# Optimization experiments

Hardware: AMD Instinct MI355X
Metric: run time of the kernel (lower is better)

Reference implementation:

```python
import jax, jax.numpy as jnp
import numpy as np

BN_EPS = 1e-5


def setup_inputs() -> dict:
    key = jax.random.key(0)
    ks = jax.random.split(key, 9)
    C = 256
    x = jax.random.normal(ks[0], (4, C, 56, 56), jnp.float32)
    Wq = jax.random.normal(ks[1], (C // 4, C), jnp.float32) * 0.05
    Wk = jax.random.normal(ks[2], (C // 4, C), jnp.float32) * 0.05
    Wv = jax.random.normal(ks[3], (C, 2 * C), jnp.float32) * 0.05
    bv = jax.random.normal(ks[4], (C,), jnp.float32) * 0.05
    gamma = jnp.ones((C,), jnp.float32)
    beta = jnp.zeros((C,), jnp.float32)
    rmean = jax.random.normal(ks[5], (C,), jnp.float32) * 0.05
    rvar = jax.random.uniform(ks[6], (C,), jnp.float32) + 0.5
    return {"x": x, "Wq": Wq, "Wk": Wk, "Wv": Wv, "bv": bv,
            "gamma": gamma, "beta": beta, "rmean": rmean, "rvar": rvar, "k": 7}


def _patches(t, k):
    # t: [b, c, h, w] -> [b, c, k*k, h, w], zero-padded neighborhoods (matches F.unfold row-major order)
    b, c, h, w = t.shape
    p = (k - 1) // 2
    tp = jnp.pad(t, ((0, 0), (0, 0), (p, p), (p, p)))
    return jnp.stack([tp[:, :, i:i + h, j:j + w] for i in range(k) for j in range(k)], axis=2)


def _align(ta, tb, k, Wq, Wk):
    b, c, h, w = ta.shape
    hw = h * w
    # query token per pixel: [b, hw, 1, c]
    spta = ta.reshape(b, c, hw).transpose(0, 2, 1)[:, :, None, :]
    # unfolded k^2 neighborhood of tb: [b, hw, k2, c]
    pt = _patches(tb, k).reshape(b, c, k * k, hw).transpose(0, 3, 2, 1)
    keys = jnp.concatenate([spta, pt], axis=2)          # [b, hw, 1+k2, c]
    q = jnp.einsum('bnqc,dc->bnqd', spta, Wq)           # [b, hw, 1, c/4]
    kk = jnp.einsum('bnkc,dc->bnkd', keys, Wk)          # [b, hw, 1+k2, c/4]
    attn = jax.nn.softmax(jnp.einsum('bnqd,bnkd->bnqk', q, kk), axis=-1)
    out = jnp.einsum('bnqk,bnkc->bnqc', attn[..., 1:], pt)  # drop self-key column
    return out[:, :, 0, :].transpose(0, 2, 1).reshape(b, c, h, w)


def reference(x, Wq, Wk, Wv, bv, gamma, beta, rmean, rvar, k):
    xt1, xt2 = jnp.split(x, 2, axis=0)
    xt1 = _align(xt2, xt1, k, Wq, Wk)   # note: second call uses the freshly aligned xt1 (as in source)
    xt2 = _align(xt1, xt2, k, Wq, Wk)
    xt = jnp.concatenate([xt1, xt2], axis=0)
    cat = jnp.concatenate([x, xt], axis=1)              # [2B, 2C, H, W]
    y = jnp.einsum('bchw,oc->bohw', cat, Wv) + bv[None, :, None, None]
    scale = (gamma / jnp.sqrt(rvar + BN_EPS))[None, :, None, None]
    y = (y - rmean[None, :, None, None]) * scale + beta[None, :, None, None]
    return jax.nn.relu(y)
```

## Files before the change

### kernel.cpp

```cpp
#include <hip/hip_runtime.h>
#include <hip/hip_bf16.h>

#define HW 3136
#define W56 56

typedef __attribute__((ext_vector_type(8))) short short8;
typedef __attribute__((ext_vector_type(4))) float f32x4;

static __device__ __forceinline__ f32x4 mfma16(short8 a, short8 b, f32x4 c) {
    return __builtin_amdgcn_mfma_f32_16x16x32_bf16(a, b, c, 0, 0, 0);
}
static __device__ __forceinline__ float b2f(unsigned short u) {
    unsigned int x = ((unsigned int)u) << 16;
    return __builtin_bit_cast(float, x);
}
static __device__ __forceinline__ unsigned short f2b(float f) {
    __hip_bfloat16 h = __float2bfloat16(f);
    return *(unsigned short*)&h;
}

__global__ __launch_bounds__(256) void prep(const float* __restrict__ x,
                                            const float* __restrict__ Wq, const float* __restrict__ Wk,
                                            const float* __restrict__ Wv,
                                            unsigned short* __restrict__ catb,
                                            unsigned short* __restrict__ xlo,
                                            unsigned short* __restrict__ Wqk_hi,
                                            unsigned short* __restrict__ Wqk_lo,
                                            unsigned short* __restrict__ Wvb) {
    __shared__ float tile[32][33];
    int bx = blockIdx.x, tid = threadIdx.x;
    if (bx < 3136) {
        int b = bx / 784, rem = bx % 784;
        int p0 = (rem >> 3) * 32, c0 = (rem & 7) * 32;
        int tx = tid & 31, ty = tid >> 5;
#pragma unroll
        for (int i = ty; i < 32; i += 8)
            tile[i][tx] = x[((size_t)b * 256 + c0 + i) * HW + p0 + tx];
        __syncthreads();
#pragma unroll
        for (int i = ty; i < 32; i += 8) {
            float v = tile[tx][i];
            unsigned short hi = f2b(v);
            unsigned short lo = f2b(v - b2f(hi));
            size_t row = (size_t)b * HW + p0 + i;
            catb[row * 512 + c0 + tx] = hi;
            xlo[row * 256 + c0 + tx] = lo;
        }
    } else {
        int i = (bx - 3136) * 256 + tid;
        if (i < 32768) {
            float w = (i < 16384) ? Wq[i] : Wk[i - 16384];
            unsigned short hi = f2b(w);
            Wqk_hi[i] = hi;
            Wqk_lo[i] = f2b(w - b2f(hi));
        }
        if (i < 131072) Wvb[i] = f2b(Wv[i]);
    }
}

__global__ __launch_bounds__(256) void projqk(const unsigned short* __restrict__ Whi,
                                              const unsigned short* __restrict__ Wlo,
                                              const unsigned short* __restrict__ Bhi_g, int bstr,
                                              const unsigned short* __restrict__ Blo_g,
                                              float* __restrict__ Qout,
                                              unsigned short* __restrict__ Kout) {
    __shared__ short Ahi[64][72], Alo[64][72];
    __shared__ short Bhi[32][72], Blo[32][72];
    int tid = threadIdx.x, lane = tid & 63, wv = tid >> 6;
    int l15 = lane & 15, lk = (lane >> 4) * 8;
    int pxb = blockIdx.x * 32;
    int y64 = blockIdx.y * 64;
    int ar0 = tid >> 3, ac = (tid & 7) * 8;
    int br = tid >> 3, bc = (tid & 7) * 8;
    f32x4 acc[2];
    acc[0] = (f32x4){0.f, 0.f, 0.f, 0.f};
    acc[1] = (f32x4){0.f, 0.f, 0.f, 0.f};

    short8 rAh0 = *(const short8*)(Whi + (size_t)(y64 + ar0) * 256 + ac);
    short8 rAl0 = *(const short8*)(Wlo + (size_t)(y64 + ar0) * 256 + ac);
    short8 rAh1 = *(const short8*)(Whi + (size_t)(y64 + ar0 + 32) * 256 + ac);
    short8 rAl1 = *(const short8*)(Wlo + (size_t)(y64 + ar0 + 32) * 256 + ac);
    short8 rBh  = *(const short8*)(Bhi_g + (size_t)(pxb + br) * bstr + bc);
    short8 rBl  = *(const short8*)(Blo_g + (size_t)(pxb + br) * 256 + bc);

#pragma unroll
    for (int t = 0; t < 4; ++t) {
        *(short8*)&Ahi[ar0][ac] = rAh0;      *(short8*)&Alo[ar0][ac] = rAl0;
        *(short8*)&Ahi[ar0 + 32][ac] = rAh1; *(short8*)&Alo[ar0 + 32][ac] = rAl1;
        *(short8*)&Bhi[br][bc] = rBh;        *(short8*)&Blo[br][bc] = rBl;
        __syncthreads();
        if (t < 3) {
            int kn = t * 64 + 64;
            rAh0 = *(const short8*)(Whi + (size_t)(y64 + ar0) * 256 + kn + ac);
            rAl0 = *(const short8*)(Wlo + (size_t)(y64 + ar0) * 256 + kn + ac);
            rAh1 = *(const short8*)(Whi + (size_t)(y64 + ar0 + 32) * 256 + kn + ac);
            rAl1 = *(const short8*)(Wlo + (size_t)(y64 + ar0 + 32) * 256 + kn + ac);
            rBh  = *(const short8*)(Bhi_g + (size_t)(pxb + br) * bstr + kn + bc);
            rBl  = *(const short8*)(Blo_g + (size_t)(pxb + br) * 256 + kn + bc);
        }
#pragma unroll
        for (int ks = 0; ks < 2; ++ks) {
            short8 ah = *(const short8*)&Ahi[wv * 16 + l15][ks * 32 + lk];
            short8 al = *(const short8*)&Alo[wv * 16 + l15][ks * 32 + lk];
            short8 bh[2], bl[2];
#pragma unroll
            for (int j = 0; j < 2; ++j) {
                bh[j] = *(const short8*)&Bhi[j * 16 + l15][ks * 32 + lk];
                bl[j] = *(const short8*)&Blo[j * 16 + l15][ks * 32 + lk];
            }
#pragma unroll
            for (int j = 0; j < 2; ++j) {
                acc[j] = mfma16(ah, bh[j], acc[j]);
                acc[j] = mfma16(ah, bl[j], acc[j]);
                acc[j] = mfma16(al, bh[j], acc[j]);
            }
        }
        __syncthreads();
    }
    int d0 = wv * 16 + (lane >> 4) * 4;
    if (blockIdx.y == 0) {
#pragma unroll
        for (int j = 0; j < 2; ++j) {
            int px = pxb + j * 16 + l15;
            *(f32x4*)(Qout + (size_t)px * 64 + d0) = acc[j];
        }
    } else {
#pragma unroll
        for (int j = 0; j < 2; ++j) {
            int px = pxb + j * 16 + l15;
            ushort4 kb;
            kb.x = f2b(acc[j][0]); kb.y = f2b(acc[j][1]);
            kb.z = f2b(acc[j][2]); kb.w = f2b(acc[j][3]);
            *(ushort4*)(Kout + (size_t)px * 64 + d0) = kb;
        }
    }
}

__global__ __launch_bounds__(256) void attn_kernel(const float* __restrict__ Q,
                                                   const unsigned short* __restrict__ Kb,
                                                   int selfOff, int kbOff,
                                                   const unsigned short* __restrict__ V,
                                                   unsigned short* __restrict__ outb,
                                                   unsigned short* __restrict__ outlo) {
    __shared__ float wsh[4][64];
    __shared__ float ls[4][52];
    __shared__ int njsh[4][64];
    int tid = threadIdx.x, lane = tid & 63, wv = tid >> 6;
    int nbc = gridDim.x >> 3;
    int lb = (blockIdx.x & 7) * nbc + (blockIdx.x >> 3);
    int gw = lb * 4 + wv;
    int b = gw / HW, pix = gw % HW;
    int py = pix / W56, px = pix % W56;

    int valid = 0, nj = 0;
    if (lane == 0) {
        valid = 1;
    } else if (lane < 50) {
        int d = lane - 1, dy = d / 7 - 3, dx = d % 7 - 3;
        int ny = py + dy, nx = px + dx;
        if (ny >= 0 && ny < W56 && nx >= 0 && nx < W56) { valid = 1; nj = ny * W56 + nx; }
    }
    njsh[wv][lane] = nj;

    int rg = lane >> 4, c = lane & 15;
    f32x4 qf = *(const f32x4*)(Q + (size_t)gw * 64 + c * 4);
    ushort4 kvv[13];
#pragma unroll
    for (int i = 0; i < 13; ++i) {
        int r = i * 4 + rg;
        int row = (i == 0 && rg == 0) ? (selfOff + gw) : (kbOff + b * HW + njsh[wv][r]);
        kvv[i] = *(const ushort4*)(Kb + (size_t)row * 64 + c * 4);
    }

    float pl[13];
#pragma unroll
    for (int i = 0; i < 13; ++i)
        pl[i] = b2f(kvv[i].x) * qf[0] + b2f(kvv[i].y) * qf[1] +
                b2f(kvv[i].z) * qf[2] + b2f(kvv[i].w) * qf[3];
#pragma unroll
    for (int off = 1; off < 16; off <<= 1)
#pragma unroll
        for (int i = 0; i < 13; ++i) pl[i] += __shfl_xor(pl[i], off);
    float myl = 0.f;
#pragma unroll
    for (int i = 0; i < 13; ++i) myl = (c == i) ? pl[i] : myl;
    if (c < 13) ls[wv][c * 4 + rg] = myl;

    float logit = (lane < 50 && valid) ? ls[wv][lane] : 0.f;
    float m = (lane < 50) ? logit : -1e30f;
#pragma unroll
    for (int off = 32; off; off >>= 1) m = fmaxf(m, __shfl_xor(m, off));
    float e = (lane < 50) ? __expf(logit - m) : 0.f;
    float s = e;
#pragma unroll
    for (int off = 32; off; off >>= 1) s += __shfl_xor(s, off);
    float w = (lane >= 1 && lane < 50 && valid) ? e / s : 0.f;
    wsh[wv][lane] = w;

    int h = lane >> 5, l32 = lane & 31;
    int jb = h * 25;
    float av[8];
#pragma unroll
    for (int cc = 0; cc < 8; ++cc) av[cc] = 0.f;
    const unsigned short* vb = V + (size_t)b * HW * 512 + l32 * 8;
#pragma unroll
    for (int g = 0; g < 2; ++g) {
        float wj[12];
        short8 vj[12];
#pragma unroll
        for (int u = 0; u < 12; ++u) {
            int j = jb + g * 12 + u;
            wj[u] = wsh[wv][j];
            vj[u] = *(const short8*)(vb + (size_t)njsh[wv][j] * 512);
        }
#pragma unroll
        for (int u = 0; u < 12; ++u)
#pragma unroll
            for (int cc = 0; cc < 8; ++cc)
                av[cc] += wj[u] * b2f((unsigned short)vj[u][cc]);
    }
    {
        int j = jb + 24;
        float wt = wsh[wv][j];
        short8 vt = *(const short8*)(vb + (size_t)njsh[wv][j] * 512);
#pragma unroll
        for (int cc = 0; cc < 8; ++cc) av[cc] += wt * b2f((unsigned short)vt[cc]);
    }
#pragma unroll
    for (int cc = 0; cc < 8; ++cc) av[cc] += __shfl_xor(av[cc], 32);

    if (h == 0) {
        short8 pk, lo8;
#pragma unroll
        for (int cc = 0; cc < 8; ++cc) {
            unsigned short hi = f2b(av[cc]);
            pk[cc] = (short)hi;
            lo8[cc] = (short)f2b(av[cc] - b2f(hi));
        }
        *(short8*)(outb + (size_t)gw * 512 + l32 * 8) = pk;
        if (outlo) *(short8*)(outlo + (size_t)gw * 256 + l32 * 8) = lo8;
    }
}

__global__ __launch_bounds__(256) void conv_mfma(const unsigned short* __restrict__ catb,
                                                 const unsigned short* __restrict__ Wvb,
                                                 const float* __restrict__ bv, const float* __restrict__ gamma,
                                                 const float* __restrict__ beta, const float* __restrict__ rmean,
                                                 const float* __restrict__ rvar, float* __restrict__ out) {
    __shared__ short Ald[64][72];
    __shared__ short Bld[64][72];
    int tid = threadIdx.x, lane = tid & 63, wv = tid >> 6;
    int wm = wv >> 1, wn = wv & 1;
    int l15 = lane & 15, lk = (lane >> 4) * 8;
    int n0g = blockIdx.x * 64;
    int m0g = blockIdx.y * 64;
    f32x4 acc[2][2];
#pragma unroll
    for (int i = 0; i < 2; ++i)
#pragma unroll
        for (int j = 0; j < 2; ++j) acc[i][j] = (f32x4){0.f, 0.f, 0.f, 0.f};

    float sc_[2][4], sh_[2][4];
#pragma unroll
    for (int i = 0; i < 2; ++i) {
        int ob = m0g + wm * 32 + i * 16 + (lane >> 4) * 4;
#pragma unroll
        for (int r = 0; r < 4; ++r) {
            int o = ob + r;
            float s = gamma[o] * rsqrtf(rvar[o] + 1e-5f);
            sc_[i][r] = s;
            sh_[i][r] = (bv[o] - rmean[o]) * s + beta[o];
        }
    }

    for (int kt = 0; kt < 512; kt += 64) {
#pragma unroll
        for (int s = 0; s < 2; ++s) {
            int q = tid + 256 * s;
            int r = q >> 3, c = (q & 7) * 8;
            *(short8*)&Ald[r][c] = *(const short8*)(Wvb + (size_t)(m0g + r) * 512 + kt + c);
            *(short8*)&Bld[r][c] = *(const short8*)(catb + (size_t)(n0g + r) * 512 + kt + c);
        }
        __syncthreads();
#pragma unroll
        for (int ks = 0; ks < 2; ++ks) {
            short8 a[2], b[2];
#pragma unroll
            for (int i = 0; i < 2; ++i) a[i] = *(const short8*)&Ald[wm * 32 + i * 16 + l15][ks * 32 + lk];
#pragma unroll
            for (int j = 0; j < 2; ++j) b[j] = *(const short8*)&Bld[wn * 32 + j * 16 + l15][ks * 32 + lk];
#pragma unroll
            for (int i = 0; i < 2; ++i)
#pragma unroll
                for (int j = 0; j < 2; ++j) acc[i][j] = mfma16(a[i], b[j], acc[i][j]);
        }
        __syncthreads();
    }
#pragma unroll
    for (int i = 0; i < 2; ++i) {
        int ob = m0g + wm * 32 + i * 16 + (lane >> 4) * 4;
#pragma unroll
        for (int j = 0; j < 2; ++j) {
            int px = n0g + wn * 32 + j * 16 + l15;
            int b = px / HW, p = px - b * HW;
            f32x4 v = acc[i][j];
#pragma unroll
            for (int r = 0; r < 4; ++r) {
                out[((size_t)(b * 256 + ob + r)) * HW + p] = fmaxf(v[r] * sc_[i][r] + sh_[i][r], 0.f);
            }
        }
    }
}

extern "C" void kernel_launch(void* const* d_in, const int* in_sizes, int n_in,
                              void* d_out, int out_size, void* d_ws, size_t ws_size,
                              hipStream_t stream) {
    const float* x     = (const float*)d_in[0];
    const float* Wq    = (const float*)d_in[1];
    const float* Wk    = (const float*)d_in[2];
    const float* Wv    = (const float*)d_in[3];
    const float* bv    = (const float*)d_in[4];
    const float* gamma = (const float*)d_in[5];
    const float* beta  = (const float*)d_in[6];
    const float* rmean = (const float*)d_in[7];
    const float* rvar  = (const float*)d_in[8];
    float* out = (float*)d_out;

    float* Qall = (float*)d_ws;
    float* Qn   = Qall + (size_t)4 * HW * 64;
    unsigned short* Kb = (unsigned short*)(Qn + (size_t)2 * HW * 64);
    unsigned short* catb   = Kb + (size_t)6 * HW * 64;
    unsigned short* xlo    = catb + (size_t)4 * HW * 512;
    unsigned short* xt1lo  = xlo + (size_t)4 * HW * 256;
    unsigned short* Wqk_hi = xt1lo + (size_t)2 * HW * 256;
    unsigned short* Wqk_lo = Wqk_hi + 128 * 256;
    unsigned short* Wvb    = Wqk_lo + 128 * 256;

    prep<<<3648, 256, 0, stream>>>(x, Wq, Wk, Wv, catb, xlo, Wqk_hi, Wqk_lo, Wvb);

    projqk<<<dim3(392, 2), 256, 0, stream>>>(Wqk_hi, Wqk_lo, catb, 512, xlo, Qall, Kb);

    attn_kernel<<<1568, 256, 0, stream>>>(Qall + (size_t)2 * HW * 64, Kb,
                                          2 * HW, 0,
                                          catb, catb + 256, xt1lo);

    projqk<<<dim3(196, 2), 256, 0, stream>>>(Wqk_hi, Wqk_lo, catb + 256, 512, xt1lo,
                                             Qn, Kb + (size_t)4 * HW * 64);

    attn_kernel<<<1568, 256, 0, stream>>>(Qn, Kb,
                                          4 * HW, 2 * HW,
                                          catb + (size_t)2 * HW * 512,
                                          catb + (size_t)2 * HW * 512 + 256, nullptr);

    conv_mfma<<<dim3(196, 4), 256, 0, stream>>>(catb, Wvb, bv, gamma, beta, rmean, rvar, out);
}
```

Baseline: 62.90 us.

## Process two adjacent pixels per wave in attention and prefetch conv tiles

The attention kernel now handles two horizontally adjacent pixels per wavefront. It builds a shared 7x8 union neighborhood, so each V row is loaded once and accumulated into both outputs with separately shifted weights. This roughly halves the gather traffic for the value aggregation and halves the grid size, at the cost of more registers and LDS. The conv GEMM also gains register prefetch of the next K tile while MFMAs run on the current one, overlapping global loads with compute.

```diff
diff --git a/kernel.cpp b/kernel.cpp
--- a/kernel.cpp
+++ b/kernel.cpp
@@ -142,104 +142,148 @@
                                                    const unsigned short* __restrict__ V,
                                                    unsigned short* __restrict__ outb,
                                                    unsigned short* __restrict__ outlo) {
-    __shared__ float wsh[4][64];
-    __shared__ float ls[4][52];
-    __shared__ int njsh[4][64];
+    __shared__ float wsh[4][2][64];
+    __shared__ float ls[4][2][52];
+    __shared__ int njs[4][2][64];
+    __shared__ int njU[4][64];
+    __shared__ float wU[4][2][64];
     int tid = threadIdx.x, lane = tid & 63, wv = tid >> 6;
     int nbc = gridDim.x >> 3;
     int lb = (blockIdx.x & 7) * nbc + (blockIdx.x >> 3);
-    int gw = lb * 4 + wv;
-    int b = gw / HW, pix = gw % HW;
-    int py = pix / W56, px = pix % W56;
-
-    int valid = 0, nj = 0;
+    int pg = lb * 8 + wv * 2;
+    int b = pg / HW, pix = pg % HW;
+    int py = pix / W56, px0 = pix % W56;
+    int gw0 = pg, gw1 = pg + 1;
+
+    int v0 = 0, n0 = 0, v1 = 0, n1 = 0;
     if (lane == 0) {
-        valid = 1;
+        v0 = 1; v1 = 1;
     } else if (lane < 50) {
         int d = lane - 1, dy = d / 7 - 3, dx = d % 7 - 3;
-        int ny = py + dy, nx = px + dx;
-        if (ny >= 0 && ny < W56 && nx >= 0 && nx < W56) { valid = 1; nj = ny * W56 + nx; }
-    }
-    njsh[wv][lane] = nj;
+        int ny = py + dy;
+        if (ny >= 0 && ny < W56) {
+            int nx0 = px0 + dx, nx1 = px0 + 1 + dx;
+            if (nx0 >= 0 && nx0 < W56) { v0 = 1; n0 = ny * W56 + nx0; }
+            if (nx1 >= 0 && nx1 < W56) { v1 = 1; n1 = ny * W56 + nx1; }
+        }
+    }
+    njs[wv][0][lane] = n0;
+    njs[wv][1][lane] = n1;
 
     int rg = lane >> 4, c = lane & 15;
-    f32x4 qf = *(const f32x4*)(Q + (size_t)gw * 64 + c * 4);
-    ushort4 kvv[13];
+    f32x4 qf0 = *(const f32x4*)(Q + (size_t)gw0 * 64 + c * 4);
+    f32x4 qf1 = *(const f32x4*)(Q + (size_t)gw1 * 64 + c * 4);
+    ushort4 kv0[13], kv1[13];
 #pragma unroll
     for (int i = 0; i < 13; ++i) {
         int r = i * 4 + rg;
-        int row = (i == 0 && rg == 0) ? (selfOff + gw) : (kbOff + b * HW + njsh[wv][r]);
-        kvv[i] = *(const ushort4*)(Kb + (size_t)row * 64 + c * 4);
-    }
-
-    float pl[13];
-#pragma unroll
-    for (int i = 0; i < 13; ++i)
-        pl[i] = b2f(kvv[i].x) * qf[0] + b2f(kvv[i].y) * qf[1] +
-                b2f(kvv[i].z) * qf[2] + b2f(kvv[i].w) * qf[3];
+        int row0 = (i == 0 && rg == 0) ? (selfOff + gw0) : (kbOff + b * HW + njs[wv][0][r]);
+        int row1 = (i == 0 && rg == 0) ? (selfOff + gw1) : (kbOff + b * HW + njs[wv][1][r]);
+        kv0[i] = *(const ushort4*)(Kb + (size_t)row0 * 64 + c * 4);
+        kv1[i] = *(const ushort4*)(Kb + (size_t)row1 * 64 + c * 4);
+    }
+
+    float pl0[13], pl1[13];
+#pragma unroll
+    for (int i = 0; i < 13; ++i) {
+        pl0[i] = b2f(kv0[i].x) * qf0[0] + b2f(kv0[i].y) * qf0[1] +
+                 b2f(kv0[i].z) * qf0[2] + b2f(kv0[i].w) * qf0[3];
+        pl1[i] = b2f(kv1[i].x) * qf1[0] + b2f(kv1[i].y) * qf1[1] +
+                 b2f(kv1[i].z) * qf1[2] + b2f(kv1[i].w) * qf1[3];
+    }
 #pragma unroll
     for (int off = 1; off < 16; off <<= 1)
 #pragma unroll
-        for (int i = 0; i < 13; ++i) pl[i] += __shfl_xor(pl[i], off);
-    float myl = 0.f;
-#pragma unroll
-    for (int i = 0; i < 13; ++i) myl = (c == i) ? pl[i] : myl;
-    if (c < 13) ls[wv][c * 4 + rg] = myl;
-
-    float logit = (lane < 50 && valid) ? ls[wv][lane] : 0.f;
-    float m = (lane < 50) ? logit : -1e30f;
-#pragma unroll
-    for (int off = 32; off; off >>= 1) m = fmaxf(m, __shfl_xor(m, off));
-    float e = (lane < 50) ? __expf(logit - m) : 0.f;
-    float s = e;
-#pragma unroll
-    for (int off = 32; off; off >>= 1) s += __shfl_xor(s, off);
-    float w = (lane >= 1 && lane < 50 && valid) ? e / s : 0.f;
-    wsh[wv][lane] = w;
+        for (int i = 0; i < 13; ++i) {
+            pl0[i] += __shfl_xor(pl0[i], off);
+            pl1[i] += __shfl_xor(pl1[i], off);
+        }
+    float my0 = 0.f, my1 = 0.f;
+#pragma unroll
+    for (int i = 0; i < 13; ++i) {
+        my0 = (c == i) ? pl0[i] : my0;
+        my1 = (c == i) ? pl1[i] : my1;
+    }
+    if (c < 13) {
+        ls[wv][0][c * 4 + rg] = my0;
+        ls[wv][1][c * 4 + rg] = my1;
+    }
+
+    float lg0 = (lane < 50 && v0) ? ls[wv][0][lane] : 0.f;
+    float lg1 = (lane < 50 && v1) ? ls[wv][1][lane] : 0.f;
+    float m0 = (lane < 50) ? lg0 : -1e30f;
+    float m1 = (lane < 50) ? lg1 : -1e30f;
+#pragma unroll
+    for (int off = 32; off; off >>= 1) {
+        m0 = fmaxf(m0, __shfl_xor(m0, off));
+        m1 = fmaxf(m1, __shfl_xor(m1, off));
+    }
+    float e0 = (lane < 50) ? __expf(lg0 - m0) : 0.f;
+    float e1 = (lane < 50) ? __expf(lg1 - m1) : 0.f;
+    float s0 = e0, s1 = e1;
+#pragma unroll
+    for (int off = 32; off; off >>= 1) {
+        s0 += __shfl_xor(s0, off);
+        s1 += __shfl_xor(s1, off);
+    }
+    wsh[wv][0][lane] = (lane >= 1 && lane < 50 && v0) ? e0 / s0 : 0.f;
+    wsh[wv][1][lane] = (lane >= 1 && lane < 50 && v1) ? e1 / s1 : 0.f;
+
+    if (lane < 56) {
+        int dy = (lane >> 3) - 3, ux = (lane & 7) - 3;
+        int ny = py + dy, nxu = px0 + ux;
+        int uv = (ny >= 0 && ny < W56 && nxu >= 0 && nxu < W56);
+        njU[wv][lane] = uv ? ny * W56 + nxu : 0;
+        float a0 = 0.f, a1 = 0.f;
+        if (ux <= 3) a0 = wsh[wv][0][1 + (dy + 3) * 7 + (ux + 3)];
+        if (ux >= -2) a1 = wsh[wv][1][1 + (dy + 3) * 7 + (ux + 2)];
+        wU[wv][0][lane] = a0;
+        wU[wv][1][lane] = a1;
+    }
 
     int h = lane >> 5, l32 = lane & 31;
-    int jb = h * 25;
-    float av[8];
-#pragma unroll
-    for (int cc = 0; cc < 8; ++cc) av[cc] = 0.f;
+    int rb = h * 28;
+    float av0[8], av1[8];
+#pragma unroll
+    for (int cc = 0; cc < 8; ++cc) { av0[cc] = 0.f; av1[cc] = 0.f; }
     const unsigned short* vb = V + (size_t)b * HW * 512 + l32 * 8;
 #pragma unroll
-    for (int g = 0; g < 2; ++g) {
-        float wj[12];
-        short8 vj[12];
-#pragma unroll
-        for (int u = 0; u < 12; ++u) {
-            int j = jb + g * 12 + u;
-            wj[u] = wsh[wv][j];
-            vj[u] = *(const short8*)(vb + (size_t)njsh[wv][j] * 512);
-        }
-#pragma unroll
-        for (int u = 0; u < 12; ++u)
-#pragma unroll
-            for (int cc = 0; cc < 8; ++cc)
-                av[cc] += wj[u] * b2f((unsigned short)vj[u][cc]);
-    }
-    {
-        int j = jb + 24;
-        float wt = wsh[wv][j];
-        short8 vt = *(const short8*)(vb + (size_t)njsh[wv][j] * 512);
-#pragma unroll
-        for (int cc = 0; cc < 8; ++cc) av[cc] += wt * b2f((unsigned short)vt[cc]);
-    }
-#pragma unroll
-    for (int cc = 0; cc < 8; ++cc) av[cc] += __shfl_xor(av[cc], 32);
-
-    if (h == 0) {
-        short8 pk, lo8;
-#pragma unroll
-        for (int cc = 0; cc < 8; ++cc) {
-            unsigned short hi = f2b(av[cc]);
-            pk[cc] = (short)hi;
-            lo8[cc] = (short)f2b(av[cc] - b2f(hi));
-        }
-        *(short8*)(outb + (size_t)gw * 512 + l32 * 8) = pk;
-        if (outlo) *(short8*)(outlo + (size_t)gw * 256 + l32 * 8) = lo8;
-    }
+    for (int g = 0; g < 4; ++g) {
+        float a0[7], a1[7];
+        short8 vj[7];
+#pragma unroll
+        for (int u = 0; u < 7; ++u) {
+            int row = rb + g * 7 + u;
+            a0[u] = wU[wv][0][row];
+            a1[u] = wU[wv][1][row];
+            vj[u] = *(const short8*)(vb + (size_t)njU[wv][row] * 512);
+        }
+#pragma unroll
+        for (int u = 0; u < 7; ++u)
+#pragma unroll
+            for (int cc = 0; cc < 8; ++cc) {
+                float vv = b2f((unsigned short)vj[u][cc]);
+                av0[cc] += a0[u] * vv;
+                av1[cc] += a1[u] * vv;
+            }
+    }
+#pragma unroll
+    for (int cc = 0; cc < 8; ++cc) {
+        av0[cc] += __shfl_xor(av0[cc], 32);
+        av1[cc] += __shfl_xor(av1[cc], 32);
+    }
+
+    short8 pk, lo8;
+#pragma unroll
+    for (int cc = 0; cc < 8; ++cc) {
+        float vvv = h ? av1[cc] : av0[cc];
+        unsigned short hi = f2b(vvv);
+        pk[cc] = (short)hi;
+        lo8[cc] = (short)f2b(vvv - b2f(hi));
+    }
+    int gww = h ? gw1 : gw0;
+    *(short8*)(outb + (size_t)gww * 512 + l32 * 8) = pk;
+    if (outlo) *(short8*)(outlo + (size_t)gww * 256 + l32 * 8) = lo8;
 }
 
 __global__ __launch_bounds__(256) void conv_mfma(const unsigned short* __restrict__ catb,
@@ -273,15 +317,25 @@
         }
     }
 
-    for (int kt = 0; kt < 512; kt += 64) {
-#pragma unroll
-        for (int s = 0; s < 2; ++s) {
-            int q = tid + 256 * s;
-            int r = q >> 3, c = (q & 7) * 8;
-            *(short8*)&Ald[r][c] = *(const short8*)(Wvb + (size_t)(m0g + r) * 512 + kt + c);
-            *(short8*)&Bld[r][c] = *(const short8*)(catb + (size_t)(n0g + r) * 512 + kt + c);
-        }
+    int r0 = tid >> 3, c0 = (tid & 7) * 8;
+    int r1 = (tid + 256) >> 3, c1 = (tid & 7) * 8;
+    short8 rA0 = *(const short8*)(Wvb + (size_t)(m0g + r0) * 512 + c0);
+    short8 rB0 = *(const short8*)(catb + (size_t)(n0g + r0) * 512 + c0);
+    short8 rA1 = *(const short8*)(Wvb + (size_t)(m0g + r1) * 512 + c1);
+    short8 rB1 = *(const short8*)(catb + (size_t)(n0g + r1) * 512 + c1);
+
+#pragma unroll
+    for (int t = 0; t < 8; ++t) {
+        *(short8*)&Ald[r0][c0] = rA0; *(short8*)&Bld[r0][c0] = rB0;
+        *(short8*)&Ald[r1][c1] = rA1; *(short8*)&Bld[r1][c1] = rB1;
         __syncthreads();
+        if (t < 7) {
+            int kn = (t + 1) * 64;
+            rA0 = *(const short8*)(Wvb + (size_t)(m0g + r0) * 512 + kn + c0);
+            rB0 = *(const short8*)(catb + (size_t)(n0g + r0) * 512 + kn + c0);
+            rA1 = *(const short8*)(Wvb + (size_t)(m0g + r1) * 512 + kn + c1);
+            rB1 = *(const short8*)(catb + (size_t)(n0g + r1) * 512 + kn + c1);
+        }
 #pragma unroll
         for (int ks = 0; ks < 2; ++ks) {
             short8 a[2], b[2];
@@ -340,17 +394,17 @@
 
     projqk<<<dim3(392, 2), 256, 0, stream>>>(Wqk_hi, Wqk_lo, catb, 512, xlo, Qall, Kb);
 
-    attn_kernel<<<1568, 256, 0, stream>>>(Qall + (size_t)2 * HW * 64, Kb,
-                                          2 * HW, 0,
-                                          catb, catb + 256, xt1lo);
+    attn_kernel<<<784, 256, 0, stream>>>(Qall + (size_t)2 * HW * 64, Kb,
+                                         2 * HW, 0,
+                                         catb, catb + 256, xt1lo);
 
     projqk<<<dim3(196, 2), 256, 0, stream>>>(Wqk_hi, Wqk_lo, catb + 256, 512, xt1lo,
                                              Qn, Kb + (size_t)4 * HW * 64);
 
-    attn_kernel<<<1568, 256, 0, stream>>>(Qn, Kb,
-                                          4 * HW, 2 * HW,
-                                          catb + (size_t)2 * HW * 512,
-                                          catb + (size_t)2 * HW * 512 + 256, nullptr);
+    attn_kernel<<<784, 256, 0, stream>>>(Qn, Kb,
+                                         4 * HW, 2 * HW,
+                                         catb + (size_t)2 * HW * 512,
+                                         catb + (size_t)2 * HW * 512 + 256, nullptr);
 
     conv_mfma<<<dim3(196, 4), 256, 0, stream>>>(catb, Wvb, bv, gamma, beta, rmean, rvar, out);
 }
```

Result: no change. 63.33 us (+0.7%).
